# Kernel optimization log

Hardware: AMD Instinct MI355X
Metric: run time of the kernel (lower is better)

The kernel has to match this reference:

```python
import jax, jax.numpy as jnp
import numpy as np

B, C, H, W_SP = 16, 128, 112, 112  # C doubles as nb_steps (time axis)
KH = 3
TAU_MEM = 1e-3
TAU_SYN = 1e-3
TIME_STEP = 1e-3
ALPHA = float(np.exp(-TIME_STEP / TAU_SYN))
BETA = float(np.exp(-TIME_STEP / TAU_MEM))


def setup_inputs() -> dict:
    key = jax.random.key(0)
    k1, k2 = jax.random.split(key)
    x = jax.random.normal(k1, (B, C, H, W_SP), dtype=jnp.float32)
    # kaiming_uniform_(a=0, mode='fan_in', nonlinearity='linear'): bound = sqrt(3) * 1/sqrt(fan_in)
    fan_in = C * KH * KH
    bound = float(np.sqrt(3.0 / fan_in))
    W = jax.random.uniform(k2, (C, C, KH, KH), minval=-bound, maxval=bound, dtype=jnp.float32)
    b = jnp.zeros((C,), dtype=jnp.float32)
    return {"x": x, "W": W, "b": b}


def reference(x, W, b):
    # Conv2d(in_channel, in_channel, kernel=3, stride=1, padding=1)
    y = jax.lax.conv_general_dilated(
        x, W, window_strides=(1, 1), padding=((1, 1), (1, 1)),
        dimension_numbers=("NCHW", "OIHW", "NCHW")) + b[None, :, None, None]
    conv_shape = y.shape
    Bsz, T = y.shape[0], y.shape[1]  # T == nb_steps (channel axis reused as time)
    X = y.reshape(Bsz, T, -1)  # (B, T, H*W)
    # FFT of leakage kernels: l = alpha^t, k = beta^t * (1 - beta)
    t = jnp.arange(T, dtype=jnp.float32)
    l = jnp.power(jnp.float32(ALPHA), t)
    k = jnp.power(jnp.float32(BETA), t) * (1.0 - jnp.float32(BETA))
    fft_l_k = jnp.fft.rfft(l, n=2 * T) * jnp.fft.rfft(k, n=2 * T)  # (T+1,)
    # Parallel leaky integration via linear (causal) convolution in frequency domain
    fft_X = jnp.fft.rfft(X, n=2 * T, axis=1)  # (B, T+1, H*W) complex
    mem = jnp.fft.irfft(fft_X * fft_l_k[None, :, None], n=2 * T, axis=1)[:, :T]
    return mem.reshape(conv_shape)
```

## Files before the change

### kernel.cpp

```cpp
#include <hip/hip_runtime.h>

typedef __attribute__((ext_vector_type(8))) short s16x8;
typedef __attribute__((ext_vector_type(8))) unsigned short u16x8;
typedef __attribute__((ext_vector_type(4))) float f32x4;

#define ALPHA_F 0.36787944117144233f
#define BETA_F  0.36787944117144233f
#define OMB_F   0.63212055882855767f

#define XS_PSTR  40
#define XS_RSTR  720
#define XS_U16   7200
#define YS_STRIDE 130

__device__ __forceinline__ unsigned short f2bf(float f){
  union { float f; unsigned int u; } v; v.f = f;
  unsigned int u = v.u;
  return (unsigned short)((u + 0x7FFFu + ((u >> 16) & 1u)) >> 16);
}
__device__ __forceinline__ float bf2f(unsigned short s){
  union { unsigned int u; float f; } v; v.u = ((unsigned int)s) << 16;
  return v.f;
}

__global__ __launch_bounds__(256) void reorder_w(const float* __restrict__ W,
                                                 unsigned short* __restrict__ Wr){
  int f = blockIdx.x * 256 + threadIdx.x;
  if (f >= 9*128*128) return;
  int cil = f & 31;
  int co  = (f >> 5) & 127;
  int cic = (f >> 12) & 3;
  int pos = f >> 14;
  int ci  = (cic << 5) | cil;
  Wr[f] = f2bf(W[(co*128 + ci)*9 + pos]);
}

__global__ __launch_bounds__(256, 3) void conv_lif(
    const float* __restrict__ x,
    const unsigned short* __restrict__ Wr,
    const float* __restrict__ bias,
    float* __restrict__ out)
{
  __shared__ unsigned short sm[128*YS_STRIDE];
  const int tid  = threadIdx.x;
  const int lane = tid & 63;
  const int wid  = tid >> 6;
  const int l15  = lane & 15;
  const int quad = lane >> 4;
  const int bz = blockIdx.z;
  const int h0 = blockIdx.y * 8, w0 = blockIdx.x * 16;

  const float* xb = x + (size_t)bz * 1605632;

  int  g_off[3], g_ci0[3];
  bool g_val[3];
  #pragma unroll
  for (int it = 0; it < 3; ++it){
    int u = tid + it*256;
    bool act = (u < 720);
    int uu = act ? u : 0;
    int pos = uu >> 2, cq = uu & 3;
    int row = pos / 18, col = pos - row*18;
    int gh = h0 - 1 + row, gw = w0 - 1 + col;
    bool val = act && (gh >= 0) && (gh < 112) && (gw >= 0) && (gw < 112);
    g_off[it] = val ? (gh*112 + gw) : 0;
    g_ci0[it] = cq << 3;
    g_val[it] = val;
  }

  u16x8 g[3];
  #define GATHER(cic_) do{ \
    _Pragma("unroll") \
    for (int it = 0; it < 3; ++it){ \
      const float* p = xb + (size_t)(g_ci0[it] + ((cic_) << 5)) * 12544 + g_off[it]; \
      u16x8 v; \
      _Pragma("unroll") \
      for (int k = 0; k < 8; ++k){ \
        float f = p[(size_t)k * 12544]; \
        f = g_val[it] ? f : 0.0f; \
        v[k] = f2bf(f); \
      } \
      g[it] = v; \
    } }while(0)

  #define WBUF(buf_) do{ \
    unsigned short* xw = sm + (buf_)*XS_U16; \
    _Pragma("unroll") \
    for (int it = 0; it < 3; ++it){ \
      int u = tid + it*256; \
      if (u < 720) *(u16x8*)(xw + (u >> 2)*XS_PSTR + ((u & 3) << 3)) = g[it]; \
    } }while(0)

  f32x4 acc[2][8];
  #pragma unroll
  for (int i = 0; i < 2; ++i)
    #pragma unroll
    for (int j = 0; j < 8; ++j) acc[i][j] = (f32x4){0.f,0.f,0.f,0.f};

  GATHER(0); WBUF(0);

  for (int cic = 0; cic < 4; ++cic){
    __syncthreads();
    const unsigned short* xs = sm + (cic & 1)*XS_U16;
    #pragma unroll
    for (int dw = 0; dw < 3; ++dw){
      s16x8 af[3][2];
      #pragma unroll
      for (int dh = 0; dh < 3; ++dh){
        const unsigned short* wp = Wr + ((((dh*3 + dw) << 2) + cic) << 12)
                                      + (((wid << 5) + l15) << 5) + (quad << 3);
        af[dh][0] = *(const s16x8*)wp;
        af[dh][1] = *(const s16x8*)(wp + 512);
      }
      const unsigned short* bcol = xs + (l15 + dw)*XS_PSTR + (quad << 3);
      s16x8 R[6];
      #pragma unroll
      for (int r = 0; r < 4; ++r) R[r] = *(const s16x8*)(bcol + r*XS_RSTR);
      #pragma unroll
      for (int p = 0; p < 4; ++p){
        if (p < 3){
          R[(2*p+4) % 6] = *(const s16x8*)(bcol + (2*p+4)*XS_RSTR);
          R[(2*p+5) % 6] = *(const s16x8*)(bcol + (2*p+5)*XS_RSTR);
        }
        #pragma unroll
        for (int dh = 0; dh < 3; ++dh){
          #pragma unroll
          for (int sub = 0; sub < 2; ++sub){
            int nt = 2*p + sub;
            s16x8 b = R[(nt + dh) % 6];
            acc[0][nt] = __builtin_amdgcn_mfma_f32_16x16x32_bf16(af[dh][0], b, acc[0][nt], 0, 0, 0);
            acc[1][nt] = __builtin_amdgcn_mfma_f32_16x16x32_bf16(af[dh][1], b, acc[1][nt], 0, 0, 0);
          }
        }
      }
      if (dw == 1 && cic < 3) GATHER(cic+1);
    }
    if (cic < 3) WBUF((cic+1) & 1);
  }

  __syncthreads();
  #pragma unroll
  for (int mt = 0; mt < 2; ++mt){
    int cobase = (wid << 5) + (mt << 4) + (quad << 2);
    float4 bv = *(const float4*)(bias + cobase);
    #pragma unroll
    for (int nt = 0; nt < 8; ++nt){
      int pix = (nt << 4) + l15;
      f32x4 a = acc[mt][nt];
      ushort2 w01, w23;
      w01.x = f2bf(a.x + bv.x);
      w01.y = f2bf(a.y + bv.y);
      w23.x = f2bf(a.z + bv.z);
      w23.y = f2bf(a.w + bv.w);
      unsigned short* yp = sm + pix*YS_STRIDE + cobase;
      *(ushort2*)(yp)     = w01;
      *(ushort2*)(yp + 2) = w23;
    }
  }
  __syncthreads();

  {
    int pix  = tid & 127;
    int half = tid >> 7;
    int r = pix >> 4, c = pix & 15;
    float s = 0.f, m = 0.f;
    float* op = out + (size_t)bz*1605632 + (h0 + r)*112 + (w0 + c);
    const unsigned short* yr = sm + pix*YS_STRIDE;
    int t0     = half ? 48 : 0;
    int tstore = half ? 64 : 0;
    int tend   = half ? 128 : 64;
    for (int t = t0; t < tend; ++t){
      float y = bf2f(yr[t]);
      s = ALPHA_F * s + y;
      m = BETA_F  * m + OMB_F * s;
      if (t >= tstore) op[(size_t)t*12544] = m;
    }
  }
  #undef GATHER
  #undef WBUF
}

extern "C" void kernel_launch(void* const* d_in, const int* in_sizes, int n_in,
                              void* d_out, int out_size, void* d_ws, size_t ws_size,
                              hipStream_t stream){
  const float* x = (const float*)d_in[0];
  const float* W = (const float*)d_in[1];
  const float* b = (const float*)d_in[2];
  float* out = (float*)d_out;
  unsigned short* Wr = (unsigned short*)d_ws;
  reorder_w<<<576, 256, 0, stream>>>(W, Wr);
  conv_lif<<<dim3(7, 14, 16), 256, 0, stream>>>(x, Wr, b, out);
}
```

Measured before the change: 266.9 us.

## Pre-convert input to padded channel-last bf16 layout before conv

Adds a separate pass that converts x to bf16 in a zero-padded, channel-innermost (32-channel chunk) layout in workspace. The conv kernel can then gather each tile with one 16-byte vector load per slot, with no strided fp32 loads, bounds checks or per-element conversion. It also raises the occupancy hint from 3 to 4 blocks per SM. The cost is an extra kernel launch plus a full read of x and a write of the half-size copy, and it falls back to the old path when the workspace is too small.

```diff
diff --git a/kernel.cpp b/kernel.cpp
--- a/kernel.cpp
+++ b/kernel.cpp
@@ -12,6 +12,9 @@
 #define XS_RSTR  720
 #define XS_U16   7200
 #define YS_STRIDE 130
+
+#define X2_CICSTR 415872u
+#define X2_BZSTR  1663488u
 
 __device__ __forceinline__ unsigned short f2bf(float f){
   union { float f; unsigned int u; } v; v.f = f;
@@ -35,8 +38,46 @@
   Wr[f] = f2bf(W[(co*128 + ci)*9 + pos]);
 }
 
-__global__ __launch_bounds__(256, 3) void conv_lif(
+__global__ __launch_bounds__(256) void convert_x(const float* __restrict__ x,
+                                                 unsigned short* __restrict__ x2){
+  __shared__ float ls[112*33 + 1];
+  const int tid = threadIdx.x;
+  const int h = blockIdx.x, cic = blockIdx.y, bz = blockIdx.z;
+  const float* src = x + ((size_t)(bz*128 + cic*32))*12544 + (size_t)h*112;
+  #pragma unroll
+  for (int r = 0; r < 7; ++r){
+    int u2 = r*256 + tid;
+    int ci = u2 / 56, w2 = (u2 - ci*56) << 1;
+    float2 v = *(const float2*)(src + (size_t)ci*12544 + w2);
+    ls[w2*33 + ci] = v.x;
+    ls[(w2+1)*33 + ci] = v.y;
+  }
+  __syncthreads();
+  unsigned short* dst = x2 + (size_t)(bz*4 + cic)*X2_CICSTR + (size_t)(h+1)*(114*32);
+  #pragma unroll
+  for (int r = 0; r < 7; ++r){
+    int u2 = r*256 + tid;
+    int pw = u2 >> 4, c2 = (u2 & 15) << 1;
+    ushort2 o;
+    o.x = f2bf(ls[pw*33 + c2]);
+    o.y = f2bf(ls[pw*33 + c2 + 1]);
+    *(ushort2*)(dst + (pw+1)*32 + c2) = o;
+  }
+  if (tid < 64){
+    int cil = tid & 31;
+    dst[((tid >> 5) ? 113*32 : 0) + cil] = 0;
+  }
+  if (h == 0 || h == 111){
+    unsigned short* brow = x2 + (size_t)(bz*4 + cic)*X2_CICSTR
+                              + (size_t)(h == 0 ? 0 : 113)*(114*32);
+    for (int u = tid; u < 114*32; u += 256) brow[u] = 0;
+  }
+}
+
+template<int MODE>
+__global__ __launch_bounds__(256, 4) void conv_lif(
     const float* __restrict__ x,
+    const unsigned short* __restrict__ x2,
     const unsigned short* __restrict__ Wr,
     const float* __restrict__ bias,
     float* __restrict__ out)
@@ -51,8 +92,9 @@
   const int h0 = blockIdx.y * 8, w0 = blockIdx.x * 16;
 
   const float* xb = x + (size_t)bz * 1605632;
-
-  int  g_off[3], g_ci0[3];
+  const unsigned short* x2b = x2 + (size_t)bz * X2_BZSTR;
+
+  int  g_off[3], g_ci0[3], g_idx[3];
   bool g_val[3];
   #pragma unroll
   for (int it = 0; it < 3; ++it){
@@ -61,26 +103,41 @@
     int uu = act ? u : 0;
     int pos = uu >> 2, cq = uu & 3;
     int row = pos / 18, col = pos - row*18;
-    int gh = h0 - 1 + row, gw = w0 - 1 + col;
-    bool val = act && (gh >= 0) && (gh < 112) && (gw >= 0) && (gw < 112);
-    g_off[it] = val ? (gh*112 + gw) : 0;
-    g_ci0[it] = cq << 3;
-    g_val[it] = val;
+    if (MODE == 0){
+      int gh = h0 - 1 + row, gw = w0 - 1 + col;
+      bool val = act && (gh >= 0) && (gh < 112) && (gw >= 0) && (gw < 112);
+      g_off[it] = val ? (gh*112 + gw) : 0;
+      g_ci0[it] = cq << 3;
+      g_val[it] = val;
+      g_idx[it] = 0;
+    } else {
+      g_idx[it] = ((h0 + row)*114 + (w0 + col))*32 + (cq << 3);
+      g_val[it] = act;
+      g_off[it] = 0; g_ci0[it] = 0;
+    }
   }
 
   u16x8 g[3];
   #define GATHER(cic_) do{ \
-    _Pragma("unroll") \
-    for (int it = 0; it < 3; ++it){ \
-      const float* p = xb + (size_t)(g_ci0[it] + ((cic_) << 5)) * 12544 + g_off[it]; \
-      u16x8 v; \
+    if (MODE == 0){ \
       _Pragma("unroll") \
-      for (int k = 0; k < 8; ++k){ \
-        float f = p[(size_t)k * 12544]; \
-        f = g_val[it] ? f : 0.0f; \
-        v[k] = f2bf(f); \
+      for (int it = 0; it < 3; ++it){ \
+        const float* p = xb + (size_t)(g_ci0[it] + ((cic_) << 5)) * 12544 + g_off[it]; \
+        u16x8 v; \
+        _Pragma("unroll") \
+        for (int k = 0; k < 8; ++k){ \
+          float f = p[(size_t)k * 12544]; \
+          f = g_val[it] ? f : 0.0f; \
+          v[k] = f2bf(f); \
+        } \
+        g[it] = v; \
       } \
-      g[it] = v; \
+    } else { \
+      _Pragma("unroll") \
+      for (int it = 0; it < 3; ++it){ \
+        if (g_val[it]) \
+          g[it] = *(const u16x8*)(x2b + (size_t)(cic_)*X2_CICSTR + g_idx[it]); \
+      } \
     } }while(0)
 
   #define WBUF(buf_) do{ \
@@ -189,5 +246,14 @@
   float* out = (float*)d_out;
   unsigned short* Wr = (unsigned short*)d_ws;
   reorder_w<<<576, 256, 0, stream>>>(W, Wr);
-  conv_lif<<<dim3(7, 14, 16), 256, 0, stream>>>(x, Wr, b, out);
-}
+
+  const size_t x2_off  = 294912;
+  const size_t x2_size = (size_t)16 * X2_BZSTR * 2;
+  if (ws_size >= x2_off + x2_size){
+    unsigned short* x2 = (unsigned short*)d_ws + x2_off/2;
+    convert_x<<<dim3(112, 4, 16), 256, 0, stream>>>(x, x2);
+    conv_lif<1><<<dim3(7, 14, 16), 256, 0, stream>>>(x, x2, Wr, b, out);
+  } else {
+    conv_lif<0><<<dim3(7, 14, 16), 256, 0, stream>>>(x, nullptr, Wr, b, out);
+  }
+}
```

Measured after the change: 268.0 us. Within noise of the previous version (+0.4%).
